# Kernel optimization log

Measured on AMD Instinct MI355X. Metric: run time of the kernel, lower is better.

The kernel has to match this reference:

```python
import jax, jax.numpy as jnp
import numpy as np

D_MODEL = 1024
N_HEADS = 16
D_K = D_MODEL // N_HEADS  # 64
D_V = D_MODEL // N_HEADS  # 64
BATCH = 2
SEQ = 2048


def setup_inputs() -> dict:
    key = jax.random.key(0)
    k_x, k_q, k_k, k_v, k_o = jax.random.split(key, 5)
    s = 1.0 / np.sqrt(D_MODEL)
    return {
        "X": jax.random.normal(k_x, (BATCH, SEQ, D_MODEL), dtype=jnp.float32),
        "W_Q": jax.random.normal(k_q, (D_MODEL, N_HEADS * D_K), dtype=jnp.float32) * s,
        "W_K": jax.random.normal(k_k, (D_MODEL, N_HEADS * D_K), dtype=jnp.float32) * s,
        "W_V": jax.random.normal(k_v, (D_MODEL, N_HEADS * D_V), dtype=jnp.float32) * s,
        "W_0": jax.random.normal(k_o, (N_HEADS * D_V, D_MODEL), dtype=jnp.float32) * s,
    }


def reference(X, W_Q, W_K, W_V, W_0):
    B, S, _ = X.shape
    # Project and split heads: [B, S, H, Dk]
    Q = (X @ W_Q).reshape(B, S, N_HEADS, D_K)
    K = (X @ W_K).reshape(B, S, N_HEADS, D_K)
    V = (X @ W_V).reshape(B, S, N_HEADS, D_V)
    # NOTE: original torch code scales by sqrt(K.shape[1]) == sqrt(seq_len),
    # not sqrt(d_k). Reproduce that exactly.
    scale = jnp.sqrt(jnp.asarray(S, dtype=X.dtype))
    scores = jnp.einsum("bqhd,bkhd->bhqk", Q, K) / scale  # [B, H, S, S]
    attn = jax.nn.softmax(scores, axis=-1)
    out = jnp.einsum("bhqk,bkhd->bqhd", attn, V)  # [B, S, H, Dv]
    return out.reshape(B, S, N_HEADS * D_V) @ W_0
```

## Files before the change

### kernel.cpp

```cpp
#include <hip/hip_runtime.h>

#define D_MODEL 1024
#define SEQ     2048
#define BATCH   2
#define NH      16

using u16 = unsigned short;
typedef __bf16 bf16x8 __attribute__((ext_vector_type(8)));
typedef float  f32x4  __attribute__((ext_vector_type(4)));
typedef short  short4v __attribute__((ext_vector_type(4)));
typedef short  short8v __attribute__((ext_vector_type(8)));

__device__ __forceinline__ u16 f2bf(float f){
  union { __bf16 h; u16 u; } v; v.h = (__bf16)f; return v.u;
}

__device__ __forceinline__ void gload_lds16(const void* g, void* l){
  __builtin_amdgcn_global_load_lds(
      (const __attribute__((address_space(1))) void*)g,
      (__attribute__((address_space(3))) void*)l, 16, 0, 0);
}

__global__ __launch_bounds__(256) void k_cvt(const float* __restrict__ in,
                                             u16* __restrict__ out, int n4){
  int i = blockIdx.x*256 + threadIdx.x;
  if (i >= n4) return;
  float4 v = ((const float4*)in)[i];
  ushort4 o; o.x=f2bf(v.x); o.y=f2bf(v.y); o.z=f2bf(v.z); o.w=f2bf(v.w);
  ((ushort4*)out)[i] = o;
}

__global__ __launch_bounds__(256) void k_cvt_w_t(
    const float* __restrict__ wq, const float* __restrict__ wk,
    const float* __restrict__ wv, const float* __restrict__ w0,
    u16* __restrict__ oq, u16* __restrict__ ok,
    u16* __restrict__ ov, u16* __restrict__ o0){
  const float* W; u16* O;
  if      (blockIdx.z==0){W=wq;O=oq;}
  else if (blockIdx.z==1){W=wk;O=ok;}
  else if (blockIdx.z==2){W=wv;O=ov;}
  else               {W=w0;O=o0;}
  __shared__ float T[64][65];
  int t = threadIdx.x;
  int r0 = t>>4, cb = (t&15)*4;
  int kt = blockIdx.y*64, nt = blockIdx.x*64;
  #pragma unroll
  for (int j=0;j<4;++j){
    int r = r0 + j*16;
    float4 v = *(const float4*)(W + (size_t)(kt + r)*1024 + nt + cb);
    T[r][cb] = v.x; T[r][cb+1] = v.y; T[r][cb+2] = v.z; T[r][cb+3] = v.w;
  }
  __syncthreads();
  #pragma unroll
  for (int j=0;j<4;++j){
    int rn = r0 + j*16;
    ushort4 o;
    o.x = f2bf(T[cb  ][rn]); o.y = f2bf(T[cb+1][rn]);
    o.z = f2bf(T[cb+2][rn]); o.w = f2bf(T[cb+3][rn]);
    *(ushort4*)(O + (size_t)(nt + rn)*1024 + kt + cb) = o;
  }
}

__global__ __launch_bounds__(256) void k_gemm_qkv(
    const u16* __restrict__ A, const u16* __restrict__ Bt,
    u16* __restrict__ Ob, float scaleQ)
{
  const int K = 1024, N = 3072;
  const int nwg = gridDim.x * gridDim.y;
  const int f = blockIdx.y * gridDim.x + blockIdx.x;
  const int sw = (f & 7) * (nwg >> 3) + (f >> 3);
  const int bxs = sw % gridDim.x, bys = sw / gridDim.x;
  const int bm = bys*128, bn = bxs*128;
  const float scl = (bn < 1024) ? scaleQ : 1.0f;
  const int lane = threadIdx.x & 63, w = threadIdx.x >> 6;
  const int hi = lane >> 4, c = lane & 15;
  const int wr = w >> 1, wc = w & 1;

  __shared__ u16 As[2][128*32];
  __shared__ u16 Bs[2][128*32];

  const int i0 = 2*w, i1 = 2*w+1;
  const int rA0 = i0*16 + (lane>>2), rA1 = i1*16 + (lane>>2);
  const int cA  = (lane&3)*8;
  const u16* aS0 = A  + (size_t)(bm + rA0)*K + cA;
  const u16* aS1 = A  + (size_t)(bm + rA1)*K + cA;
  const u16* bS0 = Bt + (size_t)(bn + rA0)*K + cA;
  const u16* bS1 = Bt + (size_t)(bn + rA1)*K + cA;

  auto stage = [&](int buf, int kk){
    gload_lds16(aS0 + kk, As[buf] + i0*512);
    gload_lds16(aS1 + kk, As[buf] + i1*512);
    gload_lds16(bS0 + kk, Bs[buf] + i0*512);
    gload_lds16(bS1 + kk, Bs[buf] + i1*512);
  };

  f32x4 acc[4][4];
  #pragma unroll
  for (int mi=0;mi<4;++mi)
    #pragma unroll
    for (int ni=0;ni<4;++ni) acc[mi][ni] = (f32x4){0.f,0.f,0.f,0.f};

  stage(0, 0);
  __syncthreads();
  int cur = 0;
  for (int kk = 0; kk < K; kk += 32){
    if (kk + 32 < K) stage(cur^1, kk + 32);
    const u16* as = As[cur];
    const u16* bs = Bs[cur];
    bf16x8 af[4], bfr[4];
    #pragma unroll
    for (int mi=0;mi<4;++mi)
      af[mi] = *(const bf16x8*)(as + (wr*64 + mi*16 + c)*32 + hi*8);
    #pragma unroll
    for (int ni=0;ni<4;++ni)
      bfr[ni] = *(const bf16x8*)(bs + (wc*64 + ni*16 + c)*32 + hi*8);
    #pragma unroll
    for (int mi=0;mi<4;++mi)
      #pragma unroll
      for (int ni=0;ni<4;++ni)
        acc[mi][ni] = __builtin_amdgcn_mfma_f32_16x16x32_bf16(af[mi], bfr[ni], acc[mi][ni], 0, 0, 0);
    __syncthreads();
    cur ^= 1;
  }
  #pragma unroll
  for (int mi=0;mi<4;++mi){
    #pragma unroll
    for (int ni=0;ni<4;++ni){
      int row = bm + wr*64 + mi*16 + hi*4;
      int col = bn + wc*64 + ni*16 + c;
      #pragma unroll
      for (int r=0;r<4;++r)
        Ob[(size_t)(row + r)*N + col] = f2bf(acc[mi][ni][r] * scl);
    }
  }
}

__global__ __launch_bounds__(256) void k_gemm_out(
    const u16* __restrict__ A, const u16* __restrict__ Bt,
    float* __restrict__ OF)
{
  const int K = 1024, N = 1024;
  const int nwg = gridDim.x * gridDim.y;
  const int f = blockIdx.y * gridDim.x + blockIdx.x;
  const int sw = (f & 7) * (nwg >> 3) + (f >> 3);
  const int bxs = sw % gridDim.x, bys = sw / gridDim.x;
  const int bm = bys*128, bn = bxs*128;
  const int lane = threadIdx.x & 63, w = threadIdx.x >> 6;
  const int hi = lane >> 4, c = lane & 15;
  const int wr = w >> 1, wc = w & 1;

  __shared__ u16 As[2][128*32];
  __shared__ u16 Bs[2][128*32];

  const int i0 = 2*w, i1 = 2*w+1;
  const int rA0 = i0*16 + (lane>>2), rA1 = i1*16 + (lane>>2);
  const int cA  = (lane&3)*8;
  const u16* aS0 = A  + (size_t)(bm + rA0)*K + cA;
  const u16* aS1 = A  + (size_t)(bm + rA1)*K + cA;
  const u16* bS0 = Bt + (size_t)(bn + rA0)*K + cA;
  const u16* bS1 = Bt + (size_t)(bn + rA1)*K + cA;

  auto stage = [&](int buf, int kk){
    gload_lds16(aS0 + kk, As[buf] + i0*512);
    gload_lds16(aS1 + kk, As[buf] + i1*512);
    gload_lds16(bS0 + kk, Bs[buf] + i0*512);
    gload_lds16(bS1 + kk, Bs[buf] + i1*512);
  };

  f32x4 acc[4][4];
  #pragma unroll
  for (int mi=0;mi<4;++mi)
    #pragma unroll
    for (int ni=0;ni<4;++ni) acc[mi][ni] = (f32x4){0.f,0.f,0.f,0.f};

  stage(0, 0);
  __syncthreads();
  int cur = 0;
  for (int kk = 0; kk < K; kk += 32){
    if (kk + 32 < K) stage(cur^1, kk + 32);
    const u16* as = As[cur];
    const u16* bs = Bs[cur];
    bf16x8 af[4], bfr[4];
    #pragma unroll
    for (int mi=0;mi<4;++mi)
      af[mi] = *(const bf16x8*)(as + (wr*64 + mi*16 + c)*32 + hi*8);
    #pragma unroll
    for (int ni=0;ni<4;++ni)
      bfr[ni] = *(const bf16x8*)(bs + (wc*64 + ni*16 + c)*32 + hi*8);
    #pragma unroll
    for (int mi=0;mi<4;++mi)
      #pragma unroll
      for (int ni=0;ni<4;++ni)
        acc[mi][ni] = __builtin_amdgcn_mfma_f32_16x16x32_bf16(af[mi], bfr[ni], acc[mi][ni], 0, 0, 0);
    __syncthreads();
    cur ^= 1;
  }
  #pragma unroll
  for (int mi=0;mi<4;++mi){
    #pragma unroll
    for (int ni=0;ni<4;++ni){
      int row = bm + wr*64 + mi*16 + hi*4;
      int col = bn + wc*64 + ni*16 + c;
      #pragma unroll
      for (int r=0;r<4;++r)
        OF[(size_t)(row + r)*N + col] = acc[mi][ni][r];
    }
  }
}

__global__ __launch_bounds__(256) void k_trans_v(const u16* __restrict__ QKV,
                                                 u16* __restrict__ Vt){
  int st = blockIdx.x, bh = blockIdx.y;
  int b = bh >> 4, h = bh & 15;
  __shared__ u16 T[64][80];
  int t = threadIdx.x;
  {
    int s = t >> 2, dc = (t & 3)*16;
    const u16* src = QKV + (size_t)(b*SEQ + st*64 + s)*3072 + 2048 + h*64 + dc;
    *(uint4*)&T[s][dc]   = *(const uint4*)(src);
    *(uint4*)&T[s][dc+8] = *(const uint4*)(src + 8);
  }
  __syncthreads();
  {
    int d = t >> 2, sc = (t & 3)*16;
    u16* dst = Vt + ((size_t)bh*64 + d)*SEQ + st*64 + sc;
    u16 vals[16];
    #pragma unroll
    for (int x=0;x<16;++x){
      int p = sc + x;
      int s = (p & 0x23) | ((p & 0x04) << 2) | ((p & 0x18) >> 1);
      vals[x] = T[s][d];
    }
    uint4 w0, w1;
    w0.x = (unsigned)vals[ 0] | ((unsigned)vals[ 1] << 16);
    w0.y = (unsigned)vals[ 2] | ((unsigned)vals[ 3] << 16);
    w0.z = (unsigned)vals[ 4] | ((unsigned)vals[ 5] << 16);
    w0.w = (unsigned)vals[ 6] | ((unsigned)vals[ 7] << 16);
    w1.x = (unsigned)vals[ 8] | ((unsigned)vals[ 9] << 16);
    w1.y = (unsigned)vals[10] | ((unsigned)vals[11] << 16);
    w1.z = (unsigned)vals[12] | ((unsigned)vals[13] << 16);
    w1.w = (unsigned)vals[14] | ((unsigned)vals[15] << 16);
    *(uint4*)(dst)     = w0;
    *(uint4*)(dst + 8) = w1;
  }
}

__global__ __launch_bounds__(512, 8) void k_attn(const u16* __restrict__ QKV,
                                                 const u16* __restrict__ Vt,
                                                 u16* __restrict__ AO)
{
  const int bh = blockIdx.x, qt = blockIdx.y;
  const int b = bh >> 4, h = bh & 15;
  const int lane = threadIdx.x & 63, w = threadIdx.x >> 6;
  const int qg = w >> 1, kh = w & 1;
  const int hi = lane >> 4, c = lane & 15;

  __shared__ u16 Ks[2][64*64];
  __shared__ u16 Vs[2][64*64];

  const size_t qrow = (size_t)(b*SEQ + qt*64 + qg*16 + c);
  const bf16x8 qf0 = *(const bf16x8*)(QKV + qrow*3072 + h*64 + hi*8);
  const bf16x8 qf1 = *(const bf16x8*)(QKV + qrow*3072 + h*64 + 32 + hi*8);

  const short4v ones4 = {(short)0x3F80,(short)0x3F80,(short)0x3F80,(short)0x3F80};

  f32x4 acc_o[4];
  #pragma unroll
  for (int n=0;n<4;++n) acc_o[n] = (f32x4){0.f,0.f,0.f,0.f};
  f32x4 acc_l = (f32x4){0.f,0.f,0.f,0.f};

  const int r = w*8 + (lane>>3);
  const int sb = ((((lane&7)*16) ^ ((lane>>3)<<4)) >> 1);
  const u16* kSrc = QKV + (size_t)(b*SEQ + r)*3072 + 1024 + h*64 + sb;
  const u16* vSrc = Vt + ((size_t)bh*64 + r)*SEQ + sb;

  auto stage = [&](int buf){
    gload_lds16(kSrc, Ks[buf] + w*512);
    gload_lds16(vSrc, Vs[buf] + w*512);
    kSrc += (size_t)64*3072; vSrc += 64;
  };

  const int swz = ((c&7)<<4);
  const char* kr0 = (const char*)&Ks[0][0] + (kh*32 + c)*128 + (( 0 + hi*16) ^ swz);
  const char* kr1 = (const char*)&Ks[0][0] + (kh*32 + c)*128 + ((64 + hi*16) ^ swz);
  const char* vr  = (const char*)&Vs[0][0] + c*128 + ((kh*64 + hi*16) ^ swz);

  auto body = [&](int buf){
    const int bo = buf*8192;
    f32x4 s0 = (f32x4){0.f,0.f,0.f,0.f};
    f32x4 s1 = (f32x4){0.f,0.f,0.f,0.f};
    bf16x8 k00 = *(const bf16x8*)(kr0 + bo);
    bf16x8 k01 = *(const bf16x8*)(kr1 + bo);
    bf16x8 k10 = *(const bf16x8*)(kr0 + bo + 2048);
    bf16x8 k11 = *(const bf16x8*)(kr1 + bo + 2048);
    __builtin_amdgcn_s_setprio(1);
    s0 = __builtin_amdgcn_mfma_f32_16x16x32_bf16(k00, qf0, s0, 0,0,0);
    s1 = __builtin_amdgcn_mfma_f32_16x16x32_bf16(k10, qf0, s1, 0,0,0);
    s0 = __builtin_amdgcn_mfma_f32_16x16x32_bf16(k01, qf1, s0, 0,0,0);
    s1 = __builtin_amdgcn_mfma_f32_16x16x32_bf16(k11, qf1, s1, 0,0,0);
    __builtin_amdgcn_s_setprio(0);

    short4v a0, a1;
    #pragma unroll
    for (int i=0;i<4;++i){
      a0[i] = (short)f2bf(__builtin_amdgcn_exp2f(s0[i]));
      a1[i] = (short)f2bf(__builtin_amdgcn_exp2f(s1[i]));
    }

    __builtin_amdgcn_s_setprio(1);
    acc_l = __builtin_amdgcn_mfma_f32_16x16x16bf16_1k(a0, ones4, acc_l, 0,0,0);
    acc_l = __builtin_amdgcn_mfma_f32_16x16x16bf16_1k(a1, ones4, acc_l, 0,0,0);
    #pragma unroll
    for (int n=0;n<4;++n){
      short8v vv = *(const short8v*)(vr + bo + n*2048);
      short4v v0 = __builtin_shufflevector(vv, vv, 0,1,2,3);
      short4v v1 = __builtin_shufflevector(vv, vv, 4,5,6,7);
      acc_o[n] = __builtin_amdgcn_mfma_f32_16x16x16bf16_1k(a0, v0, acc_o[n], 0,0,0);
      acc_o[n] = __builtin_amdgcn_mfma_f32_16x16x16bf16_1k(a1, v1, acc_o[n], 0,0,0);
    }
    __builtin_amdgcn_s_setprio(0);
  };

  stage(0);
  __syncthreads();
  #pragma unroll 1
  for (int u = 0; u < SEQ/128; ++u){
    stage(1);
    body(0);
    __syncthreads();
    if (u != SEQ/128 - 1) stage(0);
    body(1);
    __syncthreads();
  }

  float* Of = (float*)&Ks[0][0];
  float* Lf = (float*)&Vs[0][0];
  if (kh == 1){
    #pragma unroll
    for (int n=0;n<4;++n)
      #pragma unroll
      for (int i=0;i<4;++i)
        Of[qg*1024 + (hi*4+i)*64 + n*16 + c] = acc_o[n][i];
    if (c == 0){
      #pragma unroll
      for (int i=0;i<4;++i) Lf[qg*16 + hi*4 + i] = acc_l[i];
    }
  }
  __syncthreads();
  if (kh == 0){
    float inv[4];
    #pragma unroll
    for (int i=0;i<4;++i)
      inv[i] = 1.0f / (acc_l[i] + Lf[qg*16 + hi*4 + i]);
    size_t obase = (size_t)(b*SEQ + qt*64 + qg*16 + hi*4)*D_MODEL + h*64;
    #pragma unroll
    for (int i=0;i<4;++i){
      #pragma unroll
      for (int n=0;n<4;++n){
        float o = acc_o[n][i] + Of[qg*1024 + (hi*4+i)*64 + n*16 + c];
        AO[obase + (size_t)i*D_MODEL + n*16 + c] = f2bf(o * inv[i]);
      }
    }
  }
}

extern "C" void kernel_launch(void* const* d_in, const int* in_sizes, int n_in,
                              void* d_out, int out_size, void* d_ws, size_t ws_size,
                              hipStream_t stream)
{
  const float* X  = (const float*)d_in[0];
  const float* Wq = (const float*)d_in[1];
  const float* Wk = (const float*)d_in[2];
  const float* Wv = (const float*)d_in[3];
  const float* W0 = (const float*)d_in[4];
  float* out = (float*)d_out;

  char* ws = (char*)d_ws;
  const size_t MB = 1024*1024;
  u16* Xb    = (u16*)(ws);
  u16* WqkvT = (u16*)(ws +  8*MB);
  u16* W0T   = (u16*)(ws + 14*MB);
  u16* QKVb  = (u16*)(ws + 16*MB);
  u16* Vt    = (u16*)(ws + 40*MB);
  u16* AO    = Xb;

  const float scaleQ = 1.4426950408889634f / sqrtf((float)SEQ);
  const int M = BATCH*SEQ;

  k_cvt<<<dim3((M*D_MODEL/4 + 255)/256), 256, 0, stream>>>(X, Xb, M*D_MODEL/4);
  k_cvt_w_t<<<dim3(16,16,4), 256, 0, stream>>>(
      Wq, Wk, Wv, W0, WqkvT, WqkvT + 1024*1024, WqkvT + 2*1024*1024, W0T);
  k_gemm_qkv<<<dim3(3072/128, M/128), 256, 0, stream>>>(Xb, WqkvT, QKVb, scaleQ);
  k_trans_v<<<dim3(SEQ/64, BATCH*NH), 256, 0, stream>>>(QKVb, Vt);
  k_attn<<<dim3(BATCH*NH, SEQ/64), 512, 0, stream>>>(QKVb, Vt, AO);
  k_gemm_out<<<dim3(1024/128, M/128), 256, 0, stream>>>(AO, W0T, out);
}
```

Measured before the change: 127.1 us.

## Process two 16-row query tiles per wave in attention to reuse K/V fragments

Each wave now handles 32 query rows (two 16-row sub-tiles), so the attention block covers 128 queries and the grid halves along the sequence dimension. The K and V fragments loaded from LDS are reused by both sub-tiles, halving LDS reads and global K/V staging per query. In exchange each wave holds twice the accumulators, occupancy is relaxed to 4 waves per EU, and there are half as many blocks plus an extra synchronized epilogue pass.

```diff
diff --git a/kernel.cpp b/kernel.cpp
--- a/kernel.cpp
+++ b/kernel.cpp
@@ -245,7 +245,7 @@
   }
 }
 
-__global__ __launch_bounds__(512, 8) void k_attn(const u16* __restrict__ QKV,
+__global__ __launch_bounds__(512, 4) void k_attn(const u16* __restrict__ QKV,
                                                  const u16* __restrict__ Vt,
                                                  u16* __restrict__ AO)
 {
@@ -258,16 +258,20 @@
   __shared__ u16 Ks[2][64*64];
   __shared__ u16 Vs[2][64*64];
 
-  const size_t qrow = (size_t)(b*SEQ + qt*64 + qg*16 + c);
-  const bf16x8 qf0 = *(const bf16x8*)(QKV + qrow*3072 + h*64 + hi*8);
-  const bf16x8 qf1 = *(const bf16x8*)(QKV + qrow*3072 + h*64 + 32 + hi*8);
+  const size_t qbase = (size_t)(b*SEQ + qt*128 + qg*32 + c);
+  const bf16x8 qA0 = *(const bf16x8*)(QKV + (qbase     )*3072 + h*64 + hi*8);
+  const bf16x8 qA1 = *(const bf16x8*)(QKV + (qbase     )*3072 + h*64 + 32 + hi*8);
+  const bf16x8 qB0 = *(const bf16x8*)(QKV + (qbase + 16)*3072 + h*64 + hi*8);
+  const bf16x8 qB1 = *(const bf16x8*)(QKV + (qbase + 16)*3072 + h*64 + 32 + hi*8);
 
   const short4v ones4 = {(short)0x3F80,(short)0x3F80,(short)0x3F80,(short)0x3F80};
 
-  f32x4 acc_o[4];
-  #pragma unroll
-  for (int n=0;n<4;++n) acc_o[n] = (f32x4){0.f,0.f,0.f,0.f};
-  f32x4 acc_l = (f32x4){0.f,0.f,0.f,0.f};
+  f32x4 acc_o0[4], acc_o1[4];
+  #pragma unroll
+  for (int n=0;n<4;++n){ acc_o0[n] = (f32x4){0.f,0.f,0.f,0.f};
+                         acc_o1[n] = (f32x4){0.f,0.f,0.f,0.f}; }
+  f32x4 acc_l0 = (f32x4){0.f,0.f,0.f,0.f};
+  f32x4 acc_l1 = (f32x4){0.f,0.f,0.f,0.f};
 
   const int r = w*8 + (lane>>3);
   const int sb = ((((lane&7)*16) ^ ((lane>>3)<<4)) >> 1);
@@ -287,36 +291,48 @@
 
   auto body = [&](int buf){
     const int bo = buf*8192;
-    f32x4 s0 = (f32x4){0.f,0.f,0.f,0.f};
-    f32x4 s1 = (f32x4){0.f,0.f,0.f,0.f};
     bf16x8 k00 = *(const bf16x8*)(kr0 + bo);
     bf16x8 k01 = *(const bf16x8*)(kr1 + bo);
     bf16x8 k10 = *(const bf16x8*)(kr0 + bo + 2048);
     bf16x8 k11 = *(const bf16x8*)(kr1 + bo + 2048);
+    f32x4 s00 = (f32x4){0.f,0.f,0.f,0.f};
+    f32x4 s10 = (f32x4){0.f,0.f,0.f,0.f};
+    f32x4 s01 = (f32x4){0.f,0.f,0.f,0.f};
+    f32x4 s11 = (f32x4){0.f,0.f,0.f,0.f};
     __builtin_amdgcn_s_setprio(1);
-    s0 = __builtin_amdgcn_mfma_f32_16x16x32_bf16(k00, qf0, s0, 0,0,0);
-    s1 = __builtin_amdgcn_mfma_f32_16x16x32_bf16(k10, qf0, s1, 0,0,0);
-    s0 = __builtin_amdgcn_mfma_f32_16x16x32_bf16(k01, qf1, s0, 0,0,0);
-    s1 = __builtin_amdgcn_mfma_f32_16x16x32_bf16(k11, qf1, s1, 0,0,0);
+    s00 = __builtin_amdgcn_mfma_f32_16x16x32_bf16(k00, qA0, s00, 0,0,0);
+    s10 = __builtin_amdgcn_mfma_f32_16x16x32_bf16(k10, qA0, s10, 0,0,0);
+    s01 = __builtin_amdgcn_mfma_f32_16x16x32_bf16(k00, qB0, s01, 0,0,0);
+    s11 = __builtin_amdgcn_mfma_f32_16x16x32_bf16(k10, qB0, s11, 0,0,0);
+    s00 = __builtin_amdgcn_mfma_f32_16x16x32_bf16(k01, qA1, s00, 0,0,0);
+    s10 = __builtin_amdgcn_mfma_f32_16x16x32_bf16(k11, qA1, s10, 0,0,0);
+    s01 = __builtin_amdgcn_mfma_f32_16x16x32_bf16(k01, qB1, s01, 0,0,0);
+    s11 = __builtin_amdgcn_mfma_f32_16x16x32_bf16(k11, qB1, s11, 0,0,0);
     __builtin_amdgcn_s_setprio(0);
 
-    short4v a0, a1;
+    short4v a00, a10, a01, a11;
     #pragma unroll
     for (int i=0;i<4;++i){
-      a0[i] = (short)f2bf(__builtin_amdgcn_exp2f(s0[i]));
-      a1[i] = (short)f2bf(__builtin_amdgcn_exp2f(s1[i]));
+      a00[i] = (short)f2bf(__builtin_amdgcn_exp2f(s00[i]));
+      a10[i] = (short)f2bf(__builtin_amdgcn_exp2f(s10[i]));
+      a01[i] = (short)f2bf(__builtin_amdgcn_exp2f(s01[i]));
+      a11[i] = (short)f2bf(__builtin_amdgcn_exp2f(s11[i]));
     }
 
     __builtin_amdgcn_s_setprio(1);
-    acc_l = __builtin_amdgcn_mfma_f32_16x16x16bf16_1k(a0, ones4, acc_l, 0,0,0);
-    acc_l = __builtin_amdgcn_mfma_f32_16x16x16bf16_1k(a1, ones4, acc_l, 0,0,0);
+    acc_l0 = __builtin_amdgcn_mfma_f32_16x16x16bf16_1k(a00, ones4, acc_l0, 0,0,0);
+    acc_l0 = __builtin_amdgcn_mfma_f32_16x16x16bf16_1k(a10, ones4, acc_l0, 0,0,0);
+    acc_l1 = __builtin_amdgcn_mfma_f32_16x16x16bf16_1k(a01, ones4, acc_l1, 0,0,0);
+    acc_l1 = __builtin_amdgcn_mfma_f32_16x16x16bf16_1k(a11, ones4, acc_l1, 0,0,0);
     #pragma unroll
     for (int n=0;n<4;++n){
       short8v vv = *(const short8v*)(vr + bo + n*2048);
       short4v v0 = __builtin_shufflevector(vv, vv, 0,1,2,3);
       short4v v1 = __builtin_shufflevector(vv, vv, 4,5,6,7);
-      acc_o[n] = __builtin_amdgcn_mfma_f32_16x16x16bf16_1k(a0, v0, acc_o[n], 0,0,0);
-      acc_o[n] = __builtin_amdgcn_mfma_f32_16x16x16bf16_1k(a1, v1, acc_o[n], 0,0,0);
+      acc_o0[n] = __builtin_amdgcn_mfma_f32_16x16x16bf16_1k(a00, v0, acc_o0[n], 0,0,0);
+      acc_o0[n] = __builtin_amdgcn_mfma_f32_16x16x16bf16_1k(a10, v1, acc_o0[n], 0,0,0);
+      acc_o1[n] = __builtin_amdgcn_mfma_f32_16x16x16bf16_1k(a01, v0, acc_o1[n], 0,0,0);
+      acc_o1[n] = __builtin_amdgcn_mfma_f32_16x16x16bf16_1k(a11, v1, acc_o1[n], 0,0,0);
     }
     __builtin_amdgcn_s_setprio(0);
   };
@@ -340,10 +356,10 @@
     for (int n=0;n<4;++n)
       #pragma unroll
       for (int i=0;i<4;++i)
-        Of[qg*1024 + (hi*4+i)*64 + n*16 + c] = acc_o[n][i];
+        Of[qg*1024 + (hi*4+i)*64 + n*16 + c] = acc_o0[n][i];
     if (c == 0){
       #pragma unroll
-      for (int i=0;i<4;++i) Lf[qg*16 + hi*4 + i] = acc_l[i];
+      for (int i=0;i<4;++i) Lf[qg*16 + hi*4 + i] = acc_l0[i];
     }
   }
   __syncthreads();
@@ -351,13 +367,41 @@
     float inv[4];
     #pragma unroll
     for (int i=0;i<4;++i)
-      inv[i] = 1.0f / (acc_l[i] + Lf[qg*16 + hi*4 + i]);
-    size_t obase = (size_t)(b*SEQ + qt*64 + qg*16 + hi*4)*D_MODEL + h*64;
+      inv[i] = 1.0f / (acc_l0[i] + Lf[qg*16 + hi*4 + i]);
+    size_t obase = (size_t)(b*SEQ + qt*128 + qg*32 + hi*4)*D_MODEL + h*64;
     #pragma unroll
     for (int i=0;i<4;++i){
       #pragma unroll
       for (int n=0;n<4;++n){
-        float o = acc_o[n][i] + Of[qg*1024 + (hi*4+i)*64 + n*16 + c];
+        float o = acc_o0[n][i] + Of[qg*1024 + (hi*4+i)*64 + n*16 + c];
+        AO[obase + (size_t)i*D_MODEL + n*16 + c] = f2bf(o * inv[i]);
+      }
+    }
+  }
+  __syncthreads();
+  if (kh == 1){
+    #pragma unroll
+    for (int n=0;n<4;++n)
+      #pragma unroll
+      for (int i=0;i<4;++i)
+        Of[qg*1024 + (hi*4+i)*64 + n*16 + c] = acc_o1[n][i];
+    if (c == 0){
+      #pragma unroll
+      for (int i=0;i<4;++i) Lf[qg*16 + hi*4 + i] = acc_l1[i];
+    }
+  }
+  __syncthreads();
+  if (kh == 0){
+    float inv[4];
+    #pragma unroll
+    for (int i=0;i<4;++i)
+      inv[i] = 1.0f / (acc_l1[i] + Lf[qg*16 + hi*4 + i]);
+    size_t obase = (size_t)(b*SEQ + qt*128 + qg*32 + 16 + hi*4)*D_MODEL + h*64;
+    #pragma unroll
+    for (int i=0;i<4;++i){
+      #pragma unroll
+      for (int n=0;n<4;++n){
+        float o = acc_o1[n][i] + Of[qg*1024 + (hi*4+i)*64 + n*16 + c];
         AO[obase + (size_t)i*D_MODEL + n*16 + c] = f2bf(o * inv[i]);
       }
     }
@@ -392,6 +436,6 @@
       Wq, Wk, Wv, W0, WqkvT, WqkvT + 1024*1024, WqkvT + 2*1024*1024, W0T);
   k_gemm_qkv<<<dim3(3072/128, M/128), 256, 0, stream>>>(Xb, WqkvT, QKVb, scaleQ);
   k_trans_v<<<dim3(SEQ/64, BATCH*NH), 256, 0, stream>>>(QKVb, Vt);
-  k_attn<<<dim3(BATCH*NH, SEQ/64), 512, 0, stream>>>(QKVb, Vt, AO);
+  k_attn<<<dim3(BATCH*NH, SEQ/128), 512, 0, stream>>>(QKVb, Vt, AO);
   k_gemm_out<<<dim3(1024/128, M/128), 256, 0, stream>>>(AO, W0T, out);
 }
```

New measurement: 117.3 us. 1.08x faster.

## Widen attention query tile per wave and fuse input conversion kernels

Applied to the files above, without the earlier changes.

The attention kernel now uses 256 threads per block. Each wave handles 64 query rows instead of 16, so every K/V fragment loaded from LDS is reused across four query sub-tiles, and the block tile grows to 128 queries. The P·V and row-sum MFMAs switch from 16x16x16 to 16x16x32, halving that instruction count. The X conversion and the weight transpose-convert kernels are merged into one launch to save launch overhead. In exchange, register pressure is much higher (16 output accumulators plus four Q fragment pairs per lane), the grid has half as many blocks, and the epilogue runs four synchronised passes.

```diff
diff --git a/kernel.cpp b/kernel.cpp
--- a/kernel.cpp
+++ b/kernel.cpp
@@ -8,8 +8,6 @@
 using u16 = unsigned short;
 typedef __bf16 bf16x8 __attribute__((ext_vector_type(8)));
 typedef float  f32x4  __attribute__((ext_vector_type(4)));
-typedef short  short4v __attribute__((ext_vector_type(4)));
-typedef short  short8v __attribute__((ext_vector_type(8)));
 
 __device__ __forceinline__ u16 f2bf(float f){
   union { __bf16 h; u16 u; } v; v.h = (__bf16)f; return v.u;
@@ -21,29 +19,31 @@
       (__attribute__((address_space(3))) void*)l, 16, 0, 0);
 }
 
-__global__ __launch_bounds__(256) void k_cvt(const float* __restrict__ in,
-                                             u16* __restrict__ out, int n4){
-  int i = blockIdx.x*256 + threadIdx.x;
-  if (i >= n4) return;
-  float4 v = ((const float4*)in)[i];
-  ushort4 o; o.x=f2bf(v.x); o.y=f2bf(v.y); o.z=f2bf(v.z); o.w=f2bf(v.w);
-  ((ushort4*)out)[i] = o;
-}
-
-__global__ __launch_bounds__(256) void k_cvt_w_t(
+__global__ __launch_bounds__(256) void k_prep(
+    const float* __restrict__ X, u16* __restrict__ Xb,
     const float* __restrict__ wq, const float* __restrict__ wk,
     const float* __restrict__ wv, const float* __restrict__ w0,
     u16* __restrict__ oq, u16* __restrict__ ok,
-    u16* __restrict__ ov, u16* __restrict__ o0){
+    u16* __restrict__ ov, u16* __restrict__ o0)
+{
+  const int t = threadIdx.x;
+  if (blockIdx.x < 4096){
+    int i = blockIdx.x*256 + t;
+    float4 v = ((const float4*)X)[i];
+    ushort4 o; o.x=f2bf(v.x); o.y=f2bf(v.y); o.z=f2bf(v.z); o.w=f2bf(v.w);
+    ((ushort4*)Xb)[i] = o;
+    return;
+  }
+  const int bid = blockIdx.x - 4096;
+  const int z = bid >> 8, rem = bid & 255;
+  const int nt = (rem & 15)*64, kt = (rem >> 4)*64;
   const float* W; u16* O;
-  if      (blockIdx.z==0){W=wq;O=oq;}
-  else if (blockIdx.z==1){W=wk;O=ok;}
-  else if (blockIdx.z==2){W=wv;O=ov;}
-  else               {W=w0;O=o0;}
+  if      (z==0){W=wq;O=oq;}
+  else if (z==1){W=wk;O=ok;}
+  else if (z==2){W=wv;O=ov;}
+  else          {W=w0;O=o0;}
   __shared__ float T[64][65];
-  int t = threadIdx.x;
   int r0 = t>>4, cb = (t&15)*4;
-  int kt = blockIdx.y*64, nt = blockIdx.x*64;
   #pragma unroll
   for (int j=0;j<4;++j){
     int r = r0 + j*16;
@@ -245,7 +245,7 @@
   }
 }
 
-__global__ __launch_bounds__(512, 8) void k_attn(const u16* __restrict__ QKV,
+__global__ __launch_bounds__(256, 2) void k_attn(const u16* __restrict__ QKV,
                                                  const u16* __restrict__ Vt,
                                                  u16* __restrict__ AO)
 {
@@ -258,26 +258,41 @@
   __shared__ u16 Ks[2][64*64];
   __shared__ u16 Vs[2][64*64];
 
-  const size_t qrow = (size_t)(b*SEQ + qt*64 + qg*16 + c);
-  const bf16x8 qf0 = *(const bf16x8*)(QKV + qrow*3072 + h*64 + hi*8);
-  const bf16x8 qf1 = *(const bf16x8*)(QKV + qrow*3072 + h*64 + 32 + hi*8);
-
-  const short4v ones4 = {(short)0x3F80,(short)0x3F80,(short)0x3F80,(short)0x3F80};
-
-  f32x4 acc_o[4];
-  #pragma unroll
-  for (int n=0;n<4;++n) acc_o[n] = (f32x4){0.f,0.f,0.f,0.f};
-  f32x4 acc_l = (f32x4){0.f,0.f,0.f,0.f};
-
-  const int r = w*8 + (lane>>3);
+  const size_t qrow0 = (size_t)(b*SEQ + qt*128 + qg*64 + c);
+  bf16x8 qf0[4], qf1[4];
+  #pragma unroll
+  for (int s=0;s<4;++s){
+    qf0[s] = *(const bf16x8*)(QKV + (qrow0 + s*16)*3072 + h*64 + hi*8);
+    qf1[s] = *(const bf16x8*)(QKV + (qrow0 + s*16)*3072 + h*64 + 32 + hi*8);
+  }
+
+  bf16x8 ones8;
+  #pragma unroll
+  for (int j=0;j<8;++j) ones8[j] = (__bf16)1.0f;
+
+  f32x4 acc_o[4][4];
+  f32x4 acc_l[4];
+  #pragma unroll
+  for (int s=0;s<4;++s){
+    acc_l[s] = (f32x4){0.f,0.f,0.f,0.f};
+    #pragma unroll
+    for (int n=0;n<4;++n) acc_o[s][n] = (f32x4){0.f,0.f,0.f,0.f};
+  }
+
+  const int r0 = w*8 + (lane>>3);
+  const int r1 = 32 + r0;
   const int sb = ((((lane&7)*16) ^ ((lane>>3)<<4)) >> 1);
-  const u16* kSrc = QKV + (size_t)(b*SEQ + r)*3072 + 1024 + h*64 + sb;
-  const u16* vSrc = Vt + ((size_t)bh*64 + r)*SEQ + sb;
+  const u16* kS0 = QKV + (size_t)(b*SEQ + r0)*3072 + 1024 + h*64 + sb;
+  const u16* kS1 = QKV + (size_t)(b*SEQ + r1)*3072 + 1024 + h*64 + sb;
+  const u16* vS0 = Vt + ((size_t)bh*64 + r0)*SEQ + sb;
+  const u16* vS1 = Vt + ((size_t)bh*64 + r1)*SEQ + sb;
 
   auto stage = [&](int buf){
-    gload_lds16(kSrc, Ks[buf] + w*512);
-    gload_lds16(vSrc, Vs[buf] + w*512);
-    kSrc += (size_t)64*3072; vSrc += 64;
+    gload_lds16(kS0, Ks[buf] + w*512);
+    gload_lds16(kS1, Ks[buf] + 2048 + w*512);
+    gload_lds16(vS0, Vs[buf] + w*512);
+    gload_lds16(vS1, Vs[buf] + 2048 + w*512);
+    kS0 += (size_t)64*3072; kS1 += (size_t)64*3072; vS0 += 64; vS1 += 64;
   };
 
   const int swz = ((c&7)<<4);
@@ -287,38 +302,38 @@
 
   auto body = [&](int buf){
     const int bo = buf*8192;
-    f32x4 s0 = (f32x4){0.f,0.f,0.f,0.f};
-    f32x4 s1 = (f32x4){0.f,0.f,0.f,0.f};
     bf16x8 k00 = *(const bf16x8*)(kr0 + bo);
     bf16x8 k01 = *(const bf16x8*)(kr1 + bo);
     bf16x8 k10 = *(const bf16x8*)(kr0 + bo + 2048);
     bf16x8 k11 = *(const bf16x8*)(kr1 + bo + 2048);
-    __builtin_amdgcn_s_setprio(1);
-    s0 = __builtin_amdgcn_mfma_f32_16x16x32_bf16(k00, qf0, s0, 0,0,0);
-    s1 = __builtin_amdgcn_mfma_f32_16x16x32_bf16(k10, qf0, s1, 0,0,0);
-    s0 = __builtin_amdgcn_mfma_f32_16x16x32_bf16(k01, qf1, s0, 0,0,0);
-    s1 = __builtin_amdgcn_mfma_f32_16x16x32_bf16(k11, qf1, s1, 0,0,0);
-    __builtin_amdgcn_s_setprio(0);
-
-    short4v a0, a1;
-    #pragma unroll
-    for (int i=0;i<4;++i){
-      a0[i] = (short)f2bf(__builtin_amdgcn_exp2f(s0[i]));
-      a1[i] = (short)f2bf(__builtin_amdgcn_exp2f(s1[i]));
-    }
-
-    __builtin_amdgcn_s_setprio(1);
-    acc_l = __builtin_amdgcn_mfma_f32_16x16x16bf16_1k(a0, ones4, acc_l, 0,0,0);
-    acc_l = __builtin_amdgcn_mfma_f32_16x16x16bf16_1k(a1, ones4, acc_l, 0,0,0);
-    #pragma unroll
-    for (int n=0;n<4;++n){
-      short8v vv = *(const short8v*)(vr + bo + n*2048);
-      short4v v0 = __builtin_shufflevector(vv, vv, 0,1,2,3);
-      short4v v1 = __builtin_shufflevector(vv, vv, 4,5,6,7);
-      acc_o[n] = __builtin_amdgcn_mfma_f32_16x16x16bf16_1k(a0, v0, acc_o[n], 0,0,0);
-      acc_o[n] = __builtin_amdgcn_mfma_f32_16x16x16bf16_1k(a1, v1, acc_o[n], 0,0,0);
-    }
-    __builtin_amdgcn_s_setprio(0);
+    bf16x8 vv0 = *(const bf16x8*)(vr + bo);
+    bf16x8 vv1 = *(const bf16x8*)(vr + bo + 2048);
+    bf16x8 vv2 = *(const bf16x8*)(vr + bo + 4096);
+    bf16x8 vv3 = *(const bf16x8*)(vr + bo + 6144);
+    #pragma unroll
+    for (int s=0;s<4;++s){
+      f32x4 s0 = (f32x4){0.f,0.f,0.f,0.f};
+      f32x4 s1 = (f32x4){0.f,0.f,0.f,0.f};
+      __builtin_amdgcn_s_setprio(1);
+      s0 = __builtin_amdgcn_mfma_f32_16x16x32_bf16(k00, qf0[s], s0, 0,0,0);
+      s1 = __builtin_amdgcn_mfma_f32_16x16x32_bf16(k10, qf0[s], s1, 0,0,0);
+      s0 = __builtin_amdgcn_mfma_f32_16x16x32_bf16(k01, qf1[s], s0, 0,0,0);
+      s1 = __builtin_amdgcn_mfma_f32_16x16x32_bf16(k11, qf1[s], s1, 0,0,0);
+      __builtin_amdgcn_s_setprio(0);
+      bf16x8 a;
+      #pragma unroll
+      for (int i=0;i<4;++i){
+        a[i]   = (__bf16)__builtin_amdgcn_exp2f(s0[i]);
+        a[i+4] = (__bf16)__builtin_amdgcn_exp2f(s1[i]);
+      }
+      __builtin_amdgcn_s_setprio(1);
+      acc_l[s]    = __builtin_amdgcn_mfma_f32_16x16x32_bf16(a, ones8, acc_l[s], 0,0,0);
+      acc_o[s][0] = __builtin_amdgcn_mfma_f32_16x16x32_bf16(a, vv0, acc_o[s][0], 0,0,0);
+      acc_o[s][1] = __builtin_amdgcn_mfma_f32_16x16x32_bf16(a, vv1, acc_o[s][1], 0,0,0);
+      acc_o[s][2] = __builtin_amdgcn_mfma_f32_16x16x32_bf16(a, vv2, acc_o[s][2], 0,0,0);
+      acc_o[s][3] = __builtin_amdgcn_mfma_f32_16x16x32_bf16(a, vv3, acc_o[s][3], 0,0,0);
+      __builtin_amdgcn_s_setprio(0);
+    }
   };
 
   stage(0);
@@ -335,32 +350,36 @@
 
   float* Of = (float*)&Ks[0][0];
   float* Lf = (float*)&Vs[0][0];
-  if (kh == 1){
-    #pragma unroll
-    for (int n=0;n<4;++n)
+  #pragma unroll
+  for (int s=0;s<4;++s){
+    if (kh == 1){
+      #pragma unroll
+      for (int n=0;n<4;++n)
+        #pragma unroll
+        for (int i=0;i<4;++i)
+          Of[qg*1024 + (hi*4+i)*64 + n*16 + c] = acc_o[s][n][i];
+      if (c == 0){
+        #pragma unroll
+        for (int i=0;i<4;++i) Lf[qg*16 + hi*4 + i] = acc_l[s][i];
+      }
+    }
+    __syncthreads();
+    if (kh == 0){
+      float inv[4];
       #pragma unroll
       for (int i=0;i<4;++i)
-        Of[qg*1024 + (hi*4+i)*64 + n*16 + c] = acc_o[n][i];
-    if (c == 0){
-      #pragma unroll
-      for (int i=0;i<4;++i) Lf[qg*16 + hi*4 + i] = acc_l[i];
-    }
-  }
-  __syncthreads();
-  if (kh == 0){
-    float inv[4];
-    #pragma unroll
-    for (int i=0;i<4;++i)
-      inv[i] = 1.0f / (acc_l[i] + Lf[qg*16 + hi*4 + i]);
-    size_t obase = (size_t)(b*SEQ + qt*64 + qg*16 + hi*4)*D_MODEL + h*64;
-    #pragma unroll
-    for (int i=0;i<4;++i){
-      #pragma unroll
-      for (int n=0;n<4;++n){
-        float o = acc_o[n][i] + Of[qg*1024 + (hi*4+i)*64 + n*16 + c];
-        AO[obase + (size_t)i*D_MODEL + n*16 + c] = f2bf(o * inv[i]);
+        inv[i] = 1.0f / (acc_l[s][i] + Lf[qg*16 + hi*4 + i]);
+      size_t obase = (size_t)(b*SEQ + qt*128 + qg*64 + s*16 + hi*4)*D_MODEL + h*64;
+      #pragma unroll
+      for (int i=0;i<4;++i){
+        #pragma unroll
+        for (int n=0;n<4;++n){
+          float o = acc_o[s][n][i] + Of[qg*1024 + (hi*4+i)*64 + n*16 + c];
+          AO[obase + (size_t)i*D_MODEL + n*16 + c] = f2bf(o * inv[i]);
+        }
       }
     }
+    __syncthreads();
   }
 }
 
@@ -387,11 +406,11 @@
   const float scaleQ = 1.4426950408889634f / sqrtf((float)SEQ);
   const int M = BATCH*SEQ;
 
-  k_cvt<<<dim3((M*D_MODEL/4 + 255)/256), 256, 0, stream>>>(X, Xb, M*D_MODEL/4);
-  k_cvt_w_t<<<dim3(16,16,4), 256, 0, stream>>>(
-      Wq, Wk, Wv, W0, WqkvT, WqkvT + 1024*1024, WqkvT + 2*1024*1024, W0T);
+  k_prep<<<dim3(4096 + 1024), 256, 0, stream>>>(
+      X, Xb, Wq, Wk, Wv, W0,
+      WqkvT, WqkvT + 1024*1024, WqkvT + 2*1024*1024, W0T);
   k_gemm_qkv<<<dim3(3072/128, M/128), 256, 0, stream>>>(Xb, WqkvT, QKVb, scaleQ);
   k_trans_v<<<dim3(SEQ/64, BATCH*NH), 256, 0, stream>>>(QKVb, Vt);
-  k_attn<<<dim3(BATCH*NH, SEQ/64), 512, 0, stream>>>(QKVb, Vt, AO);
+  k_attn<<<dim3(BATCH*NH, SEQ/128), 256, 0, stream>>>(QKVb, Vt, AO);
   k_gemm_out<<<dim3(1024/128, M/128), 256, 0, stream>>>(AO, W0T, out);
 }
```

After: 107.2 us. 1.19x faster.
